# Kernel optimization log

Measured on AMD Instinct MI355X. Metric: run time of the kernel, lower is better.

The kernel has to match this reference:

```python
import jax, jax.numpy as jnp
import numpy as np
import math

B, N, C = 8, 1024, 256
NUM_HEAD = 4
HEAD_DIM = C // NUM_HEAD
K_NN = 5
SAMPLE_RATIO = 0.25
CLUSTER_NUM = max(math.ceil(N * SAMPLE_RATIO), 1)
EPS = 1e-6


def cluster_dpc_knn(x, cluster_num, k):
    # DPC-KNN clustering (faithful to TCFormer's cluster_dpc_knn, run under no_grad in torch)
    b, n, c = x.shape
    sq = jnp.sum(x * x, axis=-1)
    d2 = sq[:, :, None] + sq[:, None, :] - 2.0 * jnp.einsum('bic,bjc->bij', x, x)
    dist = jnp.sqrt(jnp.maximum(d2, 0.0)) / jnp.sqrt(jnp.asarray(c, x.dtype))  # (b,n,n)
    # k smallest distances per token (includes self, dist 0)
    neg_near, _ = jax.lax.top_k(-dist, k)
    dist_nearest = -neg_near
    density = jnp.exp(-jnp.mean(dist_nearest ** 2, axis=-1))  # (b,n)
    # deterministic tiny noise for tie-breaking (torch adds rand*1e-6)
    density = density + jax.random.uniform(jax.random.key(42), density.shape, dtype=density.dtype) * 1e-6
    mask = (density[:, None, :] > density[:, :, None]).astype(x.dtype)
    dist_max = jnp.max(dist.reshape(b, -1), axis=-1)[:, None, None]
    d_ind = jnp.min(dist * mask + dist_max * (1.0 - mask), axis=-1)  # distance indicator
    score = d_ind * density
    _, index_down = jax.lax.top_k(score, cluster_num)  # (b,cluster_num) cluster centers
    dist_c = jnp.take_along_axis(dist, index_down[:, :, None], axis=1)  # (b,cn,n)
    idx_cluster = jnp.argmin(dist_c, axis=1)  # (b,n)
    # ensure each center maps to its own cluster id
    bidx = jnp.arange(b)[:, None]
    idx_cluster = idx_cluster.at[bidx, index_down].set(jnp.broadcast_to(jnp.arange(cluster_num)[None, :], (b, cluster_num)))
    return idx_cluster


def setup_inputs() -> dict:
    key = jax.random.key(0)
    ks = jax.random.split(key, 6)
    w_scale = 1.0 / jnp.sqrt(jnp.asarray(C, jnp.float32))
    x_token = jax.random.normal(ks[0], (B, N, C), dtype=jnp.float32)
    Wq = jax.random.normal(ks[1], (C, C), dtype=jnp.float32) * w_scale
    Wk = jax.random.normal(ks[2], (C, C), dtype=jnp.float32) * w_scale
    Wv = jax.random.normal(ks[3], (C, C), dtype=jnp.float32) * w_scale
    Wp = jax.random.normal(ks[4], (C, C), dtype=jnp.float32) * w_scale
    bp = jax.random.normal(ks[5], (C,), dtype=jnp.float32) * 0.01
    return {"x_token": x_token, "Wq": Wq, "Wk": Wk, "Wv": Wv, "Wp": Wp, "bp": bp}


def reference(x_token, Wq, Wk, Wv, Wp, bp):
    b, n, c = x_token.shape
    scale = HEAD_DIM ** -0.5
    idx_cluster = cluster_dpc_knn(x_token, CLUSTER_NUM, K_NN)  # (b,n) int
    q = (x_token @ Wq.T).reshape(b, n, NUM_HEAD, HEAD_DIM).transpose(0, 2, 1, 3)
    k = (x_token @ Wk.T).reshape(b, n, NUM_HEAD, HEAD_DIM).transpose(0, 2, 1, 3)
    v = (x_token @ Wv.T).reshape(b, n, NUM_HEAD, HEAD_DIM).transpose(0, 2, 1, 3)
    scores = jnp.einsum('bhid,bhjd->bhij', q, k) * scale  # (b,h,n,n)
    # scatter into (b,cluster_num,n,c) + sum over clusters == mask scores by same-cluster
    same = (idx_cluster[:, :, None] == idx_cluster[:, None, :])[:, None, :, :]
    attn = jnp.where(same, scores, 0.0)
    # original: masked_fill(attn == 0, -1e9) then exp in float32
    attn = jnp.where(attn == 0.0, -1e9, attn)
    attn = jnp.exp(attn.astype(jnp.float32))
    attn = (attn + EPS / n) / (jnp.sum(attn, axis=-1, keepdims=True) + EPS)
    out = jnp.einsum('bhij,bhjd->bhid', attn, v).transpose(0, 2, 1, 3).reshape(b, n, c)
    return out @ Wp.T + bp
```

## Files before the change

kernel.cpp:

```cpp
#include <hip/hip_runtime.h>
#include <math.h>

#define B_ 8
#define N_ 1024
#define C_ 256
#define CN_ 256
#define EPS_ 1e-6f

__device__ __forceinline__ unsigned rotl32(unsigned x, int r){ return (x<<r)|(x>>(32-r)); }

__device__ float tf_noise(unsigned gid){
  unsigned c0 = (gid >= 4096u) ? gid - 4096u : gid;
  unsigned c1 = c0 + 4096u;
  const unsigned k0 = 0u, k1 = 42u;
  const unsigned ks2 = k0 ^ k1 ^ 0x1BD11BDAu;
  unsigned x0 = c0 + k0, x1 = c1 + k1;
  const int R0[4] = {13,15,26,6};
  const int R1[4] = {17,29,16,24};
  #pragma unroll
  for (int i=0;i<4;i++){ x0 += x1; x1 = rotl32(x1,R0[i]); x1 ^= x0; }
  x0 += k1; x1 += ks2 + 1u;
  #pragma unroll
  for (int i=0;i<4;i++){ x0 += x1; x1 = rotl32(x1,R1[i]); x1 ^= x0; }
  x0 += ks2; x1 += k0 + 2u;
  #pragma unroll
  for (int i=0;i<4;i++){ x0 += x1; x1 = rotl32(x1,R0[i]); x1 ^= x0; }
  x0 += k0; x1 += k1 + 3u;
  #pragma unroll
  for (int i=0;i<4;i++){ x0 += x1; x1 = rotl32(x1,R1[i]); x1 ^= x0; }
  x0 += k1; x1 += ks2 + 4u;
  #pragma unroll
  for (int i=0;i<4;i++){ x0 += x1; x1 = rotl32(x1,R0[i]); x1 ^= x0; }
  x0 += ks2; x1 += k0 + 5u;
  unsigned bits = (gid >= 4096u) ? x1 : x0;
  return __uint_as_float(0x3F800000u | (bits >> 9)) - 1.0f;
}

__global__ __launch_bounds__(256) void k_sq(const float* __restrict__ x, float* __restrict__ sq){
  int row = blockIdx.x * 4 + (threadIdx.x >> 6);
  int l = threadIdx.x & 63;
  const float* p = x + (size_t)row * C_;
  float s = 0.f;
  #pragma unroll
  for (int t=0;t<4;t++){ float v = p[l + 64*t]; s += v*v; }
  #pragma unroll
  for (int m=32;m;m>>=1) s += __shfl_xor(s, m);
  if (l==0) sq[row] = s;
}

__global__ __launch_bounds__(256) void k_trx(const float* __restrict__ src, float* __restrict__ dst){
  int z = blockIdx.z, rb = blockIdx.y*64, cb = blockIdx.x*64;
  const float* s = src + (size_t)z*N_*C_;
  float* d = dst + (size_t)z*N_*C_;
  __shared__ float t[64][65];
  int tid = threadIdx.x;
  int hr = tid>>4, c4 = (tid&15)*4;
  #pragma unroll
  for (int p=0;p<4;p++){
    int r = p*16 + hr;
    float4 v = *(const float4*)(s + (size_t)(rb+r)*C_ + cb + c4);
    t[r][c4+0]=v.x; t[r][c4+1]=v.y; t[r][c4+2]=v.z; t[r][c4+3]=v.w;
  }
  __syncthreads();
  int r4 = (tid&15)*4;
  #pragma unroll
  for (int p=0;p<4;p++){
    int c = p*16 + hr;
    *(float4*)(d + (size_t)(cb+c)*N_ + rb + r4) =
      make_float4(t[r4+0][c], t[r4+1][c], t[r4+2][c], t[r4+3][c]);
  }
}

__global__ __launch_bounds__(256) void k_trw(const float* __restrict__ s0, const float* __restrict__ s1,
                                             const float* __restrict__ s2, const float* __restrict__ s3,
                                             float* __restrict__ dst){
  int z = blockIdx.z;
  const float* s = (z==0)?s0:(z==1)?s1:(z==2)?s2:s3;
  float* d = dst + (size_t)z*C_*C_;
  int rb = blockIdx.y*64, cb = blockIdx.x*64;
  __shared__ float t[64][65];
  int tid = threadIdx.x;
  int hr = tid>>4, c4 = (tid&15)*4;
  #pragma unroll
  for (int p=0;p<4;p++){
    int r = p*16 + hr;
    float4 v = *(const float4*)(s + (size_t)(rb+r)*C_ + cb + c4);
    t[r][c4+0]=v.x; t[r][c4+1]=v.y; t[r][c4+2]=v.z; t[r][c4+3]=v.w;
  }
  __syncthreads();
  int r4 = (tid&15)*4;
  #pragma unroll
  for (int p=0;p<4;p++){
    int c = p*16 + hr;
    *(float4*)(d + (size_t)(cb+c)*C_ + rb + r4) =
      make_float4(t[r4+0][c], t[r4+1][c], t[r4+2][c], t[r4+3][c]);
  }
}

#define STAGE128(DST, SRC, LDA)                                                \
  _Pragma("unroll")                                                            \
  for (int rno=0;rno<4;rno++){                                                 \
    int l = rno*1024 + tid*4; int k = l>>7, n = l&127;                         \
    *(float4*)&DST[l] = *(const float4*)((SRC) + (size_t)(k0+k)*(LDA) + n);    \
  }

#define INNER88                                                                \
  _Pragma("unroll")                                                            \
  for (int kk=0;kk<32;kk++){                                                   \
    float4 a0 = *(const float4*)&As[kk*128 + ty*4];                            \
    float4 a1 = *(const float4*)&As[kk*128 + 64 + ty*4];                       \
    float4 b0 = *(const float4*)&Bs[kk*128 + tx*4];                            \
    float4 b1 = *(const float4*)&Bs[kk*128 + 64 + tx*4];                       \
    float av[8]={a0.x,a0.y,a0.z,a0.w,a1.x,a1.y,a1.z,a1.w};                     \
    float bv[8]={b0.x,b0.y,b0.z,b0.w,b1.x,b1.y,b1.z,b1.w};                     \
    _Pragma("unroll")                                                          \
    for (int r=0;r<8;r++)                                                      \
      _Pragma("unroll")                                                        \
      for (int c=0;c<8;c++) acc[r][c] += av[r]*bv[c];                          \
  }

__global__ __launch_bounds__(256) void k_dist6(const float* __restrict__ xT, const float* __restrict__ sq,
                                               float* __restrict__ dist){
  int b = blockIdx.z, bi = blockIdx.y, bj = blockIdx.x;
  const float* At = xT + (size_t)b*C_*N_ + bi*128;
  const float* Bt = xT + (size_t)b*C_*N_ + bj*128;
  __shared__ float As[32*128];
  __shared__ float Bs[32*128];
  int tid = threadIdx.x, tx = tid&15, ty = tid>>4;
  float acc[8][8] = {};
  for (int k0=0;k0<C_;k0+=32){
    STAGE128(As, At, N_)
    STAGE128(Bs, Bt, N_)
    __syncthreads();
    INNER88
    __syncthreads();
  }
  float sqj[8];
  #pragma unroll
  for (int cc=0;cc<2;cc++)
    #pragma unroll
    for (int c=0;c<4;c++) sqj[cc*4+c] = sq[b*N_ + bj*128 + cc*64 + tx*4 + c];
  float* dbase = dist + (size_t)b*N_*N_;
  #pragma unroll
  for (int rr=0;rr<2;rr++)
    #pragma unroll
    for (int r=0;r<4;r++){
      int i = bi*128 + rr*64 + ty*4 + r;
      float si = sq[b*N_ + i];
      #pragma unroll
      for (int cc=0;cc<2;cc++){
        float o[4];
        #pragma unroll
        for (int c=0;c<4;c++){
          float d2 = si + sqj[cc*4+c] - 2.f*acc[rr*4+r][cc*4+c];
          o[c] = sqrtf(fmaxf(d2, 0.f)) * 0.0625f;
        }
        *(float4*)(dbase + (size_t)i*N_ + bj*128 + cc*64 + tx*4) = make_float4(o[0],o[1],o[2],o[3]);
      }
    }
}

__global__ __launch_bounds__(256) void k_gemm8(const float* __restrict__ AT, const float* __restrict__ BT,
    const float* __restrict__ bias,
    float* __restrict__ Y0, float* __restrict__ Y1, float* __restrict__ Y2){
  int bj = blockIdx.x, bi = blockIdx.y;
  int z = bj>>1, col0 = (bj&1)*128;
  float* Y = (z==0)?Y0:(z==1)?Y1:Y2;
  int bb = bi>>3, n0 = (bi&7)*128;
  const float* At = AT + (size_t)bb*C_*N_ + n0;
  const float* Bt = BT + (size_t)z*C_*C_ + col0;
  __shared__ float As[32*128];
  __shared__ float Bs[32*128];
  int tid = threadIdx.x, tx = tid&15, ty = tid>>4;
  float acc[8][8] = {};
  for (int k0=0;k0<C_;k0+=32){
    STAGE128(As, At, N_)
    STAGE128(Bs, Bt, C_)
    __syncthreads();
    INNER88
    __syncthreads();
  }
  float bs[8];
  #pragma unroll
  for (int cc=0;cc<2;cc++)
    #pragma unroll
    for (int c=0;c<4;c++) bs[cc*4+c] = bias ? bias[col0 + cc*64 + tx*4 + c] : 0.f;
  #pragma unroll
  for (int rr=0;rr<2;rr++)
    #pragma unroll
    for (int r=0;r<4;r++){
      int m = bi*128 + rr*64 + ty*4 + r;
      #pragma unroll
      for (int cc=0;cc<2;cc++){
        *(float4*)(Y + (size_t)m*C_ + col0 + cc*64 + tx*4) =
          make_float4(acc[rr*4+r][cc*4+0]+bs[cc*4+0], acc[rr*4+r][cc*4+1]+bs[cc*4+1],
                      acc[rr*4+r][cc*4+2]+bs[cc*4+2], acc[rr*4+r][cc*4+3]+bs[cc*4+3]);
      }
    }
}

__global__ __launch_bounds__(256) void k_top5(const float* __restrict__ dist, float* __restrict__ density,
                                              float* __restrict__ rowmax){
  int row = blockIdx.x * 4 + (threadIdx.x >> 6);
  int l = threadIdx.x & 63;
  const float* p = dist + (size_t)row * N_;
  float t[5] = {1e30f,1e30f,1e30f,1e30f,1e30f};
  float mx = 0.f;
  #pragma unroll
  for (int q2=0;q2<16;q2++){
    float v = p[l + 64*q2];
    mx = fmaxf(mx, v);
    if (v < t[4]){
      t[4] = v;
      #pragma unroll
      for (int a=4;a>0;a--) if (t[a] < t[a-1]) { float tmp=t[a]; t[a]=t[a-1]; t[a-1]=tmp; }
    }
  }
  #pragma unroll
  for (int m=32;m;m>>=1) mx = fmaxf(mx, __shfl_xor(mx, m));
  float sumsq = 0.f;
  int hi = 0;
  #pragma unroll
  for (int a=0;a<5;a++){
    float head = (hi==0)?t[0]:(hi==1)?t[1]:(hi==2)?t[2]:(hi==3)?t[3]:(hi==4)?t[4]:1e30f;
    float m = head;
    #pragma unroll
    for (int mm=32;mm;mm>>=1) m = fminf(m, __shfl_xor(m, mm));
    sumsq += m*m;
    unsigned long long ball = __ballot(head == m);
    if (l == (__ffsll(ball) - 1)) hi++;
  }
  if (l == 0){
    float msq = sumsq / 5.0f;
    density[row] = expf(-msq) + tf_noise((unsigned)row) * 1e-6f;
    rowmax[row] = mx;
  }
}

__global__ __launch_bounds__(256) void k_bmax(const float* __restrict__ rowmax, float* __restrict__ bmax){
  int b = blockIdx.x; int t = threadIdx.x;
  float m = fmaxf(fmaxf(rowmax[b*N_+t], rowmax[b*N_+t+256]),
                  fmaxf(rowmax[b*N_+t+512], rowmax[b*N_+t+768]));
  __shared__ float s[256];
  s[t]=m; __syncthreads();
  for (int d=128; d; d>>=1){ if (t<d) s[t]=fmaxf(s[t],s[t+d]); __syncthreads(); }
  if (t==0) bmax[b]=s[0];
}

__global__ __launch_bounds__(256) void k_dind(const float* __restrict__ dist, const float* __restrict__ density,
                                              const float* __restrict__ bmax, float* __restrict__ score){
  int row = blockIdx.x * 4 + (threadIdx.x >> 6);
  int b = row >> 10;
  int l = threadIdx.x & 63;
  const float* p = dist + (size_t)row * N_;
  const float* db = density + b*N_;
  float di = density[row];
  float m = bmax[b];
  #pragma unroll
  for (int q2=0;q2<16;q2++){
    int j = l + 64*q2;
    float dj = db[j];
    if (dj > di) m = fminf(m, p[j]);
  }
  #pragma unroll
  for (int mm=32;mm;mm>>=1) m = fminf(m, __shfl_xor(m, mm));
  if (l==0) score[row] = m * di;
}

__global__ __launch_bounds__(1024) void k_top256(const float* __restrict__ score, int* __restrict__ idxdown){
  int b = blockIdx.x; int t = threadIdx.x;
  __shared__ float sv[1024];
  __shared__ int si[1024];
  float v = score[b*N_ + t];
  int i = t;
  for (int k = 2; k <= 1024; k <<= 1){
    for (int j = k >> 1; j > 0; j >>= 1){
      float v2; int i2;
      if (j >= 64){
        sv[t] = v; si[t] = i;
        __syncthreads();
        v2 = sv[t ^ j]; i2 = si[t ^ j];
        __syncthreads();
      } else {
        v2 = __shfl_xor(v, j);
        i2 = __shfl_xor(i, j);
      }
      bool islo = (t & j) == 0;
      float lov = islo ? v : v2,  hiv = islo ? v2 : v;
      int   loi = islo ? i : i2,  hii = islo ? i2 : i;
      bool prec = (lov > hiv) || (lov == hiv && loi < hii);
      bool up = ((t & k) == 0);
      bool dosw = up ? !prec : prec;
      if (dosw){ v = v2; i = i2; }
    }
  }
  if (t < CN_) idxdown[b*CN_ + t] = i;
}

__global__ __launch_bounds__(256) void k_assign2(const float* __restrict__ dist, const int* __restrict__ idxdown,
                                                 int* __restrict__ idxclu){
  int b = blockIdx.y;
  int jl = threadIdx.x & 31;
  int ch = threadIdx.x >> 5;
  int j = blockIdx.x*32 + jl;
  __shared__ int cen[256];
  __shared__ float sd[8][32];
  __shared__ int sk[8][32];
  cen[threadIdx.x] = idxdown[b*CN_ + threadIdx.x];
  __syncthreads();
  const float* dbase = dist + (size_t)b*N_*N_;
  float best = 1e30f; int bk = 0;
  #pragma unroll 8
  for (int kk=0; kk<32; kk++){
    int k = ch*32 + kk;
    float d = dbase[(size_t)cen[k]*N_ + j];
    if (d < best){ best = d; bk = k; }
  }
  sd[ch][jl] = best; sk[ch][jl] = bk;
  __syncthreads();
  if (ch == 0){
    #pragma unroll
    for (int c2=1;c2<8;c2++){
      float d = sd[c2][jl];
      if (d < best){ best = d; bk = sk[c2][jl]; }
    }
    idxclu[b*N_ + j] = bk;
  }
}

__global__ __launch_bounds__(256) void k_build2(const int* __restrict__ idxdown, int* __restrict__ idxclu,
                                                int* __restrict__ off, int* __restrict__ cnt,
                                                int* __restrict__ members){
  int b = blockIdx.x; int t = threadIdx.x;
  idxclu[b*N_ + idxdown[b*CN_ + t]] = t;
  __syncthreads();
  __shared__ int sc[256], so[256];
  sc[t] = 0;
  __syncthreads();
  int cl[4];
  #pragma unroll
  for (int i=0;i<4;i++){
    cl[i] = idxclu[b*N_ + i*256 + t];
    atomicAdd(&sc[cl[i]], 1);
  }
  __syncthreads();
  int mine = sc[t];
  so[t] = mine;
  __syncthreads();
  for (int d=1; d<256; d<<=1){
    int v2 = 0;
    if (t>=d) v2 = so[t-d];
    __syncthreads();
    if (t>=d) so[t] += v2;
    __syncthreads();
  }
  int excl = so[t] - mine;
  off[b*CN_+t] = excl;
  cnt[b*CN_+t] = mine;
  sc[t] = excl;
  __syncthreads();
  #pragma unroll
  for (int i=0;i<4;i++){
    int p = atomicAdd(&sc[cl[i]], 1);
    members[b*N_ + p] = i*256 + t;
  }
}

__global__ __launch_bounds__(256) void k_vsum1(const float* __restrict__ v, float* __restrict__ vsp){
  int p = blockIdx.x;
  int b = p >> 4, s = p & 15;
  int c = threadIdx.x;
  float acc = 0.f;
  const float* base = v + ((size_t)b*N_ + s*64)*C_ + c;
  #pragma unroll 8
  for (int i=0;i<64;i++) acc += base[(size_t)i*C_];
  vsp[(size_t)p*C_ + c] = acc;
}

__global__ __launch_bounds__(256) void k_vsum2(const float* __restrict__ vsp, float* __restrict__ vsum){
  int b = blockIdx.x; int c = threadIdx.x;
  float s = 0.f;
  #pragma unroll
  for (int i=0;i<16;i++) s += vsp[((size_t)b*16 + i)*C_ + c];
  vsum[b*C_ + c] = s;
}

__global__ __launch_bounds__(256) void k_attn(const float* __restrict__ q, const float* __restrict__ kmat,
                                              const float* __restrict__ v, const float* __restrict__ vsum,
                                              const int* __restrict__ idxclu, const int* __restrict__ off,
                                              const int* __restrict__ cnt, const int* __restrict__ members,
                                              float* __restrict__ att){
  int bi = blockIdx.x;
  int b = bi >> 10;
  int h = threadIdx.x >> 6, l = threadIdx.x & 63;
  int c = idxclu[bi];
  int o = off[b*CN_ + c], m = cnt[b*CN_ + c];
  int ch = h*64 + l;
  float qv = q[(size_t)bi*C_ + ch];
  float acc = 0.f, den = 0.f;
  const int* mem = members + b*N_ + o;
  for (int t=0;t<m;t++){
    int j = mem[t];
    size_t base = ((size_t)(b*N_ + j))*C_ + ch;
    float p = qv * kmat[base];
    #pragma unroll
    for (int mm=32;mm;mm>>=1) p += __shfl_xor(p, mm);
    float s = p * 0.125f;
    float e = (s == 0.0f) ? 0.0f : expf(s);
    den += e;
    acc += e * v[base];
  }
  float outv = (acc + (EPS_/1024.0f) * vsum[b*C_ + ch]) / (den + EPS_);
  att[(size_t)bi*C_ + ch] = outv;
}

extern "C" void kernel_launch(void* const* d_in, const int* in_sizes, int n_in,
                              void* d_out, int out_size, void* d_ws, size_t ws_size,
                              hipStream_t stream){
  const float* x  = (const float*)d_in[0];
  const float* Wq = (const float*)d_in[1];
  const float* Wk = (const float*)d_in[2];
  const float* Wv = (const float*)d_in[3];
  const float* Wp = (const float*)d_in[4];
  const float* bp = (const float*)d_in[5];
  float* out = (float*)d_out;

  float* ws = (float*)d_ws;
  float* dist    = ws;
  float* q       = dist + (size_t)B_*N_*N_;
  float* kk      = q    + (size_t)B_*N_*C_;
  float* v       = kk   + (size_t)B_*N_*C_;
  float* att     = v    + (size_t)B_*N_*C_;
  float* WT      = att  + (size_t)B_*N_*C_;
  float* vsp     = WT + 4*C_*C_;
  float* vsum    = vsp + 128*C_;
  float* sq      = vsum + B_*C_;
  float* rowmax  = sq + B_*N_;
  float* bmax    = rowmax + B_*N_;
  float* density = bmax + 16;
  float* score   = density + B_*N_;
  int* idxdown   = (int*)(score + B_*N_);
  int* idxclu    = idxdown + B_*CN_;
  int* cnt       = idxclu + B_*N_;
  int* off       = cnt + B_*CN_;
  int* members   = off + B_*CN_;

  float* xT   = att;
  float* attT = dist;

  k_trx<<<dim3(4,16,8),256,0,stream>>>(x, xT);
  k_trw<<<dim3(4,4,4),256,0,stream>>>(Wq, Wk, Wv, Wp, WT);
  k_sq<<<B_*N_/4,256,0,stream>>>(x, sq);
  k_dist6<<<dim3(8,8,8),256,0,stream>>>(xT, sq, dist);
  k_top5<<<B_*N_/4,256,0,stream>>>(dist, density, rowmax);
  k_bmax<<<8,256,0,stream>>>(rowmax, bmax);
  k_dind<<<B_*N_/4,256,0,stream>>>(dist, density, bmax, score);
  k_top256<<<8,1024,0,stream>>>(score, idxdown);
  k_assign2<<<dim3(32,8),256,0,stream>>>(dist, idxdown, idxclu);
  k_build2<<<8,256,0,stream>>>(idxdown, idxclu, off, cnt, members);
  k_gemm8<<<dim3(6,64),256,0,stream>>>(xT, WT, nullptr, q, kk, v);
  k_vsum1<<<128,256,0,stream>>>(v, vsp);
  k_vsum2<<<8,256,0,stream>>>(vsp, vsum);
  k_attn<<<B_*N_,256,0,stream>>>(q, kk, v, vsum, idxclu, off, cnt, members, att);
  k_trx<<<dim3(4,16,8),256,0,stream>>>(att, attT);
  k_gemm8<<<dim3(2,64),256,0,stream>>>(attT, WT + 3*C_*C_, bp, out, out, out);
}
```

Measured before the change: 319.6 us.

## Double-buffer GEMM LDS tiles with async global_load_lds staging

```diff
diff --git a/kernel.cpp b/kernel.cpp
--- a/kernel.cpp
+++ b/kernel.cpp
@@ -97,20 +97,25 @@
   }
 }
 
-#define STAGE128(DST, SRC, LDA)                                                \
+#define GLD16(GSRC, LDST)                                                      \
+  __builtin_amdgcn_global_load_lds(                                            \
+    (const __attribute__((address_space(1))) unsigned int*)(GSRC),             \
+    (__attribute__((address_space(3))) unsigned int*)(LDST), 16, 0, 0)
+
+#define STAGE16(BUF, SRC, LDA, K0)                                             \
   _Pragma("unroll")                                                            \
-  for (int rno=0;rno<4;rno++){                                                 \
-    int l = rno*1024 + tid*4; int k = l>>7, n = l&127;                         \
-    *(float4*)&DST[l] = *(const float4*)((SRC) + (size_t)(k0+k)*(LDA) + n);    \
-  }
-
-#define INNER88                                                                \
+  for (int f=0; f<2; f++){                                                     \
+    int l = f*1024 + tid*4; int k = l>>7, n = l&127;                           \
+    GLD16((SRC) + (size_t)((K0)+k)*(LDA) + n, &BUF[l]);                        \
+  }
+
+#define INNER16(AS, BS)                                                        \
   _Pragma("unroll")                                                            \
-  for (int kk=0;kk<32;kk++){                                                   \
-    float4 a0 = *(const float4*)&As[kk*128 + ty*4];                            \
-    float4 a1 = *(const float4*)&As[kk*128 + 64 + ty*4];                       \
-    float4 b0 = *(const float4*)&Bs[kk*128 + tx*4];                            \
-    float4 b1 = *(const float4*)&Bs[kk*128 + 64 + tx*4];                       \
+  for (int kk=0;kk<16;kk++){                                                   \
+    float4 a0 = *(const float4*)&AS[kk*128 + ty*4];                            \
+    float4 a1 = *(const float4*)&AS[kk*128 + 64 + ty*4];                       \
+    float4 b0 = *(const float4*)&BS[kk*128 + tx*4];                            \
+    float4 b1 = *(const float4*)&BS[kk*128 + 64 + tx*4];                       \
     float av[8]={a0.x,a0.y,a0.z,a0.w,a1.x,a1.y,a1.z,a1.w};                     \
     float bv[8]={b0.x,b0.y,b0.z,b0.w,b1.x,b1.y,b1.z,b1.w};                     \
     _Pragma("unroll")                                                          \
@@ -119,22 +124,31 @@
       for (int c=0;c<8;c++) acc[r][c] += av[r]*bv[c];                          \
   }
 
-__global__ __launch_bounds__(256) void k_dist6(const float* __restrict__ xT, const float* __restrict__ sq,
+#define KLOOP_DBUF(ASRC, LDA, BSRC, LDB)                                       \
+  STAGE16(As0, ASRC, LDA, 0) STAGE16(Bs0, BSRC, LDB, 0)                        \
+  __syncthreads();                                                             \
+  _Pragma("unroll 1")                                                          \
+  for (int tt=0; tt<8; ++tt){                                                  \
+    int t0 = tt*2;                                                             \
+    STAGE16(As1, ASRC, LDA, (t0+1)*16) STAGE16(Bs1, BSRC, LDB, (t0+1)*16)      \
+    INNER16(As0, Bs0)                                                          \
+    __syncthreads();                                                           \
+    if (t0+2 < 16){ STAGE16(As0, ASRC, LDA, (t0+2)*16)                         \
+                    STAGE16(Bs0, BSRC, LDB, (t0+2)*16) }                       \
+    INNER16(As1, Bs1)                                                          \
+    __syncthreads();                                                           \
+  }
+
+__global__ __launch_bounds__(256) void k_dist7(const float* __restrict__ xT, const float* __restrict__ sq,
                                                float* __restrict__ dist){
   int b = blockIdx.z, bi = blockIdx.y, bj = blockIdx.x;
   const float* At = xT + (size_t)b*C_*N_ + bi*128;
   const float* Bt = xT + (size_t)b*C_*N_ + bj*128;
-  __shared__ float As[32*128];
-  __shared__ float Bs[32*128];
+  __shared__ float As0[16*128], As1[16*128];
+  __shared__ float Bs0[16*128], Bs1[16*128];
   int tid = threadIdx.x, tx = tid&15, ty = tid>>4;
   float acc[8][8] = {};
-  for (int k0=0;k0<C_;k0+=32){
-    STAGE128(As, At, N_)
-    STAGE128(Bs, Bt, N_)
-    __syncthreads();
-    INNER88
-    __syncthreads();
-  }
+  KLOOP_DBUF(At, N_, Bt, N_)
   float sqj[8];
   #pragma unroll
   for (int cc=0;cc<2;cc++)
@@ -160,26 +174,21 @@
     }
 }
 
-__global__ __launch_bounds__(256) void k_gemm8(const float* __restrict__ AT, const float* __restrict__ BT,
-    const float* __restrict__ bias,
+__global__ __launch_bounds__(256) void k_gemm9(const float* __restrict__ AT, const float* __restrict__ BT,
+    const float* __restrict__ bias, int zdiv,
     float* __restrict__ Y0, float* __restrict__ Y1, float* __restrict__ Y2){
   int bj = blockIdx.x, bi = blockIdx.y;
-  int z = bj>>1, col0 = (bj&1)*128;
+  int z, col0;
+  if (zdiv){ z = bj>>1; col0 = (bj&1)*128; } else { z = 0; col0 = bj*128; }
   float* Y = (z==0)?Y0:(z==1)?Y1:Y2;
   int bb = bi>>3, n0 = (bi&7)*128;
   const float* At = AT + (size_t)bb*C_*N_ + n0;
   const float* Bt = BT + (size_t)z*C_*C_ + col0;
-  __shared__ float As[32*128];
-  __shared__ float Bs[32*128];
+  __shared__ float As0[16*128], As1[16*128];
+  __shared__ float Bs0[16*128], Bs1[16*128];
   int tid = threadIdx.x, tx = tid&15, ty = tid>>4;
   float acc[8][8] = {};
-  for (int k0=0;k0<C_;k0+=32){
-    STAGE128(As, At, N_)
-    STAGE128(Bs, Bt, C_)
-    __syncthreads();
-    INNER88
-    __syncthreads();
-  }
+  KLOOP_DBUF(At, N_, Bt, C_)
   float bs[8];
   #pragma unroll
   for (int cc=0;cc<2;cc++)
@@ -451,17 +460,17 @@
   k_trx<<<dim3(4,16,8),256,0,stream>>>(x, xT);
   k_trw<<<dim3(4,4,4),256,0,stream>>>(Wq, Wk, Wv, Wp, WT);
   k_sq<<<B_*N_/4,256,0,stream>>>(x, sq);
-  k_dist6<<<dim3(8,8,8),256,0,stream>>>(xT, sq, dist);
+  k_dist7<<<dim3(8,8,8),256,0,stream>>>(xT, sq, dist);
   k_top5<<<B_*N_/4,256,0,stream>>>(dist, density, rowmax);
   k_bmax<<<8,256,0,stream>>>(rowmax, bmax);
   k_dind<<<B_*N_/4,256,0,stream>>>(dist, density, bmax, score);
   k_top256<<<8,1024,0,stream>>>(score, idxdown);
   k_assign2<<<dim3(32,8),256,0,stream>>>(dist, idxdown, idxclu);
   k_build2<<<8,256,0,stream>>>(idxdown, idxclu, off, cnt, members);
-  k_gemm8<<<dim3(6,64),256,0,stream>>>(xT, WT, nullptr, q, kk, v);
+  k_gemm9<<<dim3(6,64),256,0,stream>>>(xT, WT, nullptr, 1, q, kk, v);
   k_vsum1<<<128,256,0,stream>>>(v, vsp);
   k_vsum2<<<8,256,0,stream>>>(vsp, vsum);
   k_attn<<<B_*N_,256,0,stream>>>(q, kk, v, vsum, idxclu, off, cnt, members, att);
   k_trx<<<dim3(4,16,8),256,0,stream>>>(att, attT);
-  k_gemm8<<<dim3(2,64),256,0,stream>>>(attT, WT + 3*C_*C_, bp, out, out, out);
-}
+  k_gemm9<<<dim3(2,64),256,0,stream>>>(attT, WT + 3*C_*C_, bp, 0, out, out, out);
+}
```

Result: slower. 367.2 us (+14.9%).
